# Performance work log

Hardware: AMD Instinct MI355X
Metric: run time of the kernel (lower is better)

## Reference

```python
import jax, jax.numpy as jnp
import numpy as np

EPS = 1e-5

def _conv3x3(x, w, b):
    y = jax.lax.conv_general_dilated(x, w, window_strides=(1, 1),
                                     padding=((1, 1), (1, 1)),
                                     dimension_numbers=('NCHW', 'OIHW', 'NCHW'))
    return y + b[None, :, None, None]

def _bilinear_gather(x, py, px):
    # x: [B,C,H,W]; py,px: [B,K,H,W] absolute sampling coords; zero outside image (DCN convention).
    B, C, H, W = x.shape
    Kk = py.shape[1]
    y0 = jnp.floor(py)
    x0 = jnp.floor(px)
    ly = py - y0
    lx = px - x0
    y0i = y0.astype(jnp.int32)
    x0i = x0.astype(jnp.int32)
    xf = x.reshape(B, C, H * W)

    def gather(yi, xi):
        valid = (yi >= 0) & (yi < H) & (xi >= 0) & (xi < W)
        idx = (jnp.clip(yi, 0, H - 1) * W + jnp.clip(xi, 0, W - 1)).reshape(B, -1)
        g = jax.vmap(lambda xb, ib: xb[:, ib])(xf, idx).reshape(B, C, Kk, H, W)
        return g * valid[:, None].astype(x.dtype)

    v00 = gather(y0i, x0i)
    v01 = gather(y0i, x0i + 1)
    v10 = gather(y0i + 1, x0i)
    v11 = gather(y0i + 1, x0i + 1)
    ly = ly[:, None]
    lx = lx[:, None]
    return (v00 * (1 - ly) * (1 - lx) + v01 * (1 - ly) * lx
            + v10 * ly * (1 - lx) + v11 * ly * lx)

def _shift_forward(x, w_off, b_off, w_conv, b_conv, gamma, beta, run_mean, run_var):
    B, C, H, W = x.shape
    om = _conv3x3(x, w_off, b_off)              # [B,27,H,W] offset/mask predictor
    dy = om[:, 0:18:2]                          # [B,9,H,W] per-tap y offsets
    dx = om[:, 1:18:2]                          # [B,9,H,W] per-tap x offsets
    mask = jax.nn.sigmoid(om[:, 18:27])         # [B,9,H,W] modulation (DCNv2)
    kk = jnp.arange(3, dtype=x.dtype) - 1.0     # kernel tap offsets for 3x3, dilation 1
    ky = jnp.repeat(kk, 3)                      # [9]
    kx = jnp.tile(kk, 3)                        # [9]
    hh = jnp.arange(H, dtype=x.dtype)
    ww = jnp.arange(W, dtype=x.dtype)
    py = hh[None, None, :, None] + ky[None, :, None, None] + dy
    px = ww[None, None, None, :] + kx[None, :, None, None] + dx
    s = _bilinear_gather(x, py, px) * mask[:, None]   # [B,C,9,H,W]
    Co = w_conv.shape[0]
    y = jnp.einsum('bckhw,ock->bohw', s, w_conv.reshape(Co, C, 9))
    y = y + b_conv[None, :, None, None]
    # BatchNorm2d (inference) + ReLU, then residual add
    inv = jax.lax.rsqrt(run_var + EPS)
    y = (y - run_mean[None, :, None, None]) * (inv * gamma)[None, :, None, None] + beta[None, :, None, None]
    y = jax.nn.relu(y)
    return x + y

def setup_inputs():
    key = jax.random.key(0)
    ks = jax.random.split(key, 3)
    B, C, H, W = 2, 256, 96, 96
    x = jax.random.normal(ks[0], (B, C, H, W), dtype=jnp.float32)
    w_off = jax.random.normal(ks[1], (27, C, 3, 3), dtype=jnp.float32) * 0.01
    b_off = jnp.zeros((27,), dtype=jnp.float32)
    w_conv = jax.random.normal(ks[2], (C, C, 3, 3), dtype=jnp.float32) * 0.02
    b_conv = jnp.zeros((C,), dtype=jnp.float32)
    gamma = jnp.ones((C,), dtype=jnp.float32)
    beta = jnp.zeros((C,), dtype=jnp.float32)
    run_mean = jnp.zeros((C,), dtype=jnp.float32)
    run_var = jnp.ones((C,), dtype=jnp.float32)
    return {"x": x, "w_off": w_off, "b_off": b_off, "w_conv": w_conv,
            "b_conv": b_conv, "gamma": gamma, "beta": beta,
            "run_mean": run_mean, "run_var": run_var}

def reference(x, w_off, b_off, w_conv, b_conv, gamma, beta, run_mean, run_var):
    return _shift_forward(x, w_off, b_off, w_conv, b_conv, gamma, beta, run_mean, run_var)
```

## Files before the change

### kernel.cpp

```cpp
#include <hip/hip_runtime.h>
#include <hip/hip_bf16.h>

#define H_ 96
#define W_ 96
#define HW_ 9216
#define C_ 256
#define B_ 2
#define KO_ 27
#define NPX_ 18432
#define EPS_ 1e-5f

typedef unsigned short u16;
typedef unsigned short ushort8 __attribute__((ext_vector_type(8)));
typedef short short8v __attribute__((ext_vector_type(8)));
typedef float float4v __attribute__((ext_vector_type(4)));

__device__ __forceinline__ float b2f(u16 u) {
    return __uint_as_float(((unsigned int)u) << 16);
}
__device__ __forceinline__ u16 f2b(float f) {
    __hip_bfloat16 h = __float2bfloat16(f);
    union { __hip_bfloat16 h; u16 u; } cv; cv.h = h; return cv.u;
}
__device__ __forceinline__ unsigned int pack2(float a, float b) {
    union { __hip_bfloat162 h; unsigned int u; } cv;
    cv.h = __float22bfloat162_rn(make_float2(a, b));
    return cv.u;
}
__device__ __forceinline__ void glds16(const u16* g, u16* l) {
    __builtin_amdgcn_global_load_lds(
        (const __attribute__((address_space(1))) void*)g,
        (__attribute__((address_space(3))) void*)l, 16, 0, 0);
}

__global__ __launch_bounds__(256) void prep_w_kernel(
    const float* __restrict__ w_conv, const float* __restrict__ w_off,
    const float* __restrict__ b_conv,
    const float* __restrict__ gamma, const float* __restrict__ beta,
    const float* __restrict__ rmean, const float* __restrict__ rvar,
    float* __restrict__ AB, u16* __restrict__ WQ, u16* __restrict__ WO)
{
    if (blockIdx.x == 0) {
        int o = threadIdx.x;
        float sc = gamma[o] * rsqrtf(rvar[o] + EPS_);
        AB[o] = sc;
        AB[256 + o] = beta[o] + (b_conv[o] - rmean[o]) * sc;
    }
    if (blockIdx.x < 2304) {
        int idx = blockIdx.x * 256 + threadIdx.x;
        int ch = idx >> 13;
        int o  = (idx >> 5) & 255;
        int cp = idx & 31;
        int c  = ((ch & 7) << 5) + cp;
        int k  = ch >> 3;
        WQ[idx] = f2b(w_conv[(o * C_ + c) * 9 + k]);
    } else {
        int j = (blockIdx.x - 2304) * 256 + threadIdx.x;
        int ch = j >> 10;
        int o  = (j >> 5) & 31;
        int cp = j & 31;
        int c  = ((ch & 7) << 5) + cp;
        int k  = ch >> 3;
        WO[j] = (o < KO_) ? f2b(w_off[(o * C_ + c) * 9 + k]) : (u16)0;
    }
}

__global__ __launch_bounds__(256) void xt_kernel(const float* __restrict__ x,
                                                 u16* __restrict__ XT)
{
    __shared__ u16 ls[32][100];
    int h  = blockIdx.x;
    int cg = blockIdx.y & 7;
    int b  = blockIdx.y >> 3;
    int c0 = cg * 32;
    for (int e = threadIdx.x; e < 32 * W_; e += 256) {
        int ci = e / W_, w = e % W_;
        ls[ci][w] = f2b(x[((b * C_ + c0 + ci) * H_ + h) * W_ + w]);
    }
    __syncthreads();
    for (int e = threadIdx.x; e < 32 * W_; e += 256) {
        int w = e >> 5, ci = e & 31;
        XT[((b * H_ + h) * W_ + w) * C_ + c0 + ci] = ls[ci][w];
    }
}

__global__ __launch_bounds__(256) void offsets_kernel(
    const u16* __restrict__ XT, const u16* __restrict__ WO,
    const float* __restrict__ b_off, float* __restrict__ OFF)
{
    __shared__ float red[4][32][16];

    const int tid = threadIdx.x;
    const int b  = blockIdx.y;
    const int p0 = blockIdx.x * 16;
    const int h  = p0 / W_;
    const int w0 = p0 % W_;

    const int wave = tid >> 6;
    const int lane = tid & 63;
    const int quad = lane >> 4;
    const int l15  = lane & 15;

    {
        const int pw = w0 + l15;
        float4v acc0 = float4v{0.f,0.f,0.f,0.f};
        float4v acc1 = float4v{0.f,0.f,0.f,0.f};
        int basec = 0; bool vld = true; int curtap = -1;
        auto set_tap = [&](int tap) {
            int py  = h + tap / 3 - 1;
            int pxl = pw + tap % 3 - 1;
            vld = ((unsigned)py < (unsigned)H_) && ((unsigned)pxl < (unsigned)W_);
            int pyc = min(max(py, 0), H_ - 1);
            int pxc = min(max(pxl, 0), W_ - 1);
            basec = ((b * H_ + pyc) * W_ + pxc) * C_ + quad * 8;
        };
        auto bload = [&](int c32) -> ushort8 {
            ushort8 v = *(const ushort8*)(XT + basec + (c32 & 7) * 32);
#pragma unroll
            for (int j = 0; j < 8; j++) v[j] = vld ? v[j] : (u16)0;
            return v;
        };
        const int c0 = wave * 18, c1 = c0 + 18;
        curtap = c0 >> 3;
        set_tap(curtap);
        ushort8 bq = bload(c0);
        short8v wa = *(const short8v*)(WO + c0 * 1024 + l15 * 32 + quad * 8);
        short8v wb = *(const short8v*)(WO + c0 * 1024 + l15 * 32 + quad * 8 + 512);
        for (int i = c0; i < c1; ++i) {
            ushort8 bc = bq;
            short8v wac = wa, wbc = wb;
            int nx = i + 1;
            if (nx < c1) {
                int t = nx >> 3;
                if (t != curtap) { set_tap(t); curtap = t; }
                bq = bload(nx);
                wa = *(const short8v*)(WO + nx * 1024 + l15 * 32 + quad * 8);
                wb = *(const short8v*)(WO + nx * 1024 + l15 * 32 + quad * 8 + 512);
            }
            union { ushort8 u; short8v s; } cb; cb.u = bc;
            acc0 = __builtin_amdgcn_mfma_f32_16x16x32_bf16(wac, cb.s, acc0, 0, 0, 0);
            acc1 = __builtin_amdgcn_mfma_f32_16x16x32_bf16(wbc, cb.s, acc1, 0, 0, 0);
        }
#pragma unroll
        for (int r = 0; r < 4; ++r) {
            red[wave][quad * 4 + r][l15]      = acc0[r];
            red[wave][16 + quad * 4 + r][l15] = acc1[r];
        }
    }
    __syncthreads();
    const int n_base = b * HW_ + p0;
#pragma unroll
    for (int rep = 0; rep < 2; ++rep) {
        int o  = (tid >> 4) + rep * 16;
        int px = tid & 15;
        if (o < KO_) {
            float v = red[0][o][px] + red[1][o][px] + red[2][o][px] + red[3][o][px]
                    + b_off[o];
            OFF[(size_t)(n_base + px) * 32 + o] =
                (o < 18) ? v : 1.f / (1.f + expf(-v));
        }
    }
}

__global__ __launch_bounds__(256) void fused_kernel(
    const float* __restrict__ x, const u16* __restrict__ XT,
    const float* __restrict__ OFF, const u16* __restrict__ WQ,
    const float* __restrict__ AB, float* __restrict__ out)
{
    __shared__ __align__(16) u16 sA[2 * 256 * 32];
    __shared__ __align__(16) u16 sB[2 * 32 * 32];
    __shared__ float offv[32][32];

    const int tid = threadIdx.x;
    const int wave = tid >> 6;
    const int lane = tid & 63;
    const int quad = lane >> 4;
    const int l15  = lane & 15;

    const int bid = blockIdx.x;
    const int swz = (bid & 7) * 72 + (bid >> 3);
    const int n0  = swz * 32;
    const int b   = n0 / HW_;
    const int p0  = n0 - b * HW_;
    const int h   = p0 / W_;
    const int w0  = p0 % W_;

    {
        int px = tid >> 3, q4 = (tid & 7) * 4;
        float4 v = *(const float4*)(OFF + (size_t)(n0 + px) * 32 + q4);
        *(float4*)&offv[px][q4] = v;
    }
    __syncthreads();

    float4v acc[4][2];
#pragma unroll
    for (int i = 0; i < 4; i++)
#pragma unroll
        for (int jj = 0; jj < 2; jj++)
            acc[i][jj] = float4v{0.f, 0.f, 0.f, 0.f};

    const int le8 = lane * 8;
    const int wo  = wave * 64;

    const int ppx = tid >> 3;
    const int pj  = tid & 7;
    const int pcc = pj >> 2;
    const int sboff = pcc * 1024 + ppx * 32 + (pj & 3) * 8;

    float fw0 = 0.f, fw1 = 0.f, fw2 = 0.f, fw3 = 0.f;
    int a00 = 0, a01 = 0, a10 = 0, a11 = 0;

#pragma unroll 4
    for (int ch = 0; ch < 36; ++ch) {
        const int tap = ch >> 2, q = ch & 3;
        if (q == 0) {
            float dy = offv[ppx][2 * tap];
            float dx = offv[ppx][2 * tap + 1];
            float m  = offv[ppx][18 + tap];
            float py  = (float)(h + tap / 3 - 1) + dy;
            float pxx = (float)(w0 + ppx + tap % 3 - 1) + dx;
            float y0f = floorf(py), x0f = floorf(pxx);
            float ly = py - y0f, lx = pxx - x0f;
            int y0 = (int)y0f, x0i = (int)x0f;
            int y1 = y0 + 1, x1 = x0i + 1;
            bool vy0 = (unsigned)y0 < (unsigned)H_;
            bool vy1 = (unsigned)y1 < (unsigned)H_;
            bool vx0 = (unsigned)x0i < (unsigned)W_;
            bool vx1 = (unsigned)x1 < (unsigned)W_;
            fw0 = (vy0 && vx0) ? (1.f - ly) * (1.f - lx) * m : 0.f;
            fw1 = (vy0 && vx1) ? (1.f - ly) * lx * m : 0.f;
            fw2 = (vy1 && vx0) ? ly * (1.f - lx) * m : 0.f;
            fw3 = (vy1 && vx1) ? ly * lx * m : 0.f;
            int y0c = min(max(y0, 0), H_ - 1), y1c = min(max(y1, 0), H_ - 1);
            int x0c = min(max(x0i, 0), W_ - 1), x1c = min(max(x1, 0), W_ - 1);
            a00 = ((b * H_ + y0c) * W_ + x0c) * C_;
            a01 = ((b * H_ + y0c) * W_ + x1c) * C_;
            a10 = ((b * H_ + y1c) * W_ + x0c) * C_;
            a11 = ((b * H_ + y1c) * W_ + x1c) * C_;
        }

        const int cbase = q * 64 + pj * 8;
        ushort8 v00 = *(const ushort8*)(XT + a00 + cbase);
        ushort8 v01 = *(const ushort8*)(XT + a01 + cbase);
        ushort8 v10 = *(const ushort8*)(XT + a10 + cbase);
        ushort8 v11 = *(const ushort8*)(XT + a11 + cbase);

#pragma unroll
        for (int i = 0; i < 8; ++i) {
            int unit = i * 4 + wave;
            int cc = unit >> 4;
            const u16* g = WQ + (size_t)(tap * 8 + q * 2 + cc) * 8192
                         + (unit & 15) * 512 + le8;
            glds16(g, &sA[unit * 512]);
        }

        {
            float v[8];
#pragma unroll
            for (int t = 0; t < 8; t++)
                v[t] = fw0 * b2f(v00[t]) + fw1 * b2f(v01[t])
                     + fw2 * b2f(v10[t]) + fw3 * b2f(v11[t]);
            uint4 sv;
            sv.x = pack2(v[0], v[1]);
            sv.y = pack2(v[2], v[3]);
            sv.z = pack2(v[4], v[5]);
            sv.w = pack2(v[6], v[7]);
            *(uint4*)&sB[sboff] = sv;
        }
        __syncthreads();

#pragma unroll
        for (int cc = 0; cc < 2; ++cc) {
            short8v af[4], bf[2];
#pragma unroll
            for (int mt = 0; mt < 4; ++mt)
                af[mt] = *(const short8v*)
                    &sA[cc * 8192 + (wo + mt * 16 + l15) * 32 + quad * 8];
#pragma unroll
            for (int nt = 0; nt < 2; ++nt)
                bf[nt] = *(const short8v*)
                    &sB[cc * 1024 + (nt * 16 + l15) * 32 + quad * 8];
#pragma unroll
            for (int mt = 0; mt < 4; ++mt)
#pragma unroll
                for (int nt = 0; nt < 2; ++nt)
                    acc[mt][nt] = __builtin_amdgcn_mfma_f32_16x16x32_bf16(
                        af[mt], bf[nt], acc[mt][nt], 0, 0, 0);
        }
        __syncthreads();
    }

    const float* Ao = AB;
    const float* Bo = AB + 256;
#pragma unroll
    for (int mt = 0; mt < 4; mt++) {
#pragma unroll
        for (int nt = 0; nt < 2; nt++) {
            int pix = p0 + nt * 16 + l15;
#pragma unroll
            for (int r = 0; r < 4; r++) {
                int o = wo + mt * 16 + quad * 4 + r;
                float v = acc[mt][nt][r] * Ao[o] + Bo[o];
                v = fmaxf(v, 0.f);
                int gi = (b * C_ + o) * HW_ + pix;
                out[gi] = x[gi] + v;
            }
        }
    }
}

extern "C" void kernel_launch(void* const* d_in, const int* in_sizes, int n_in,
                              void* d_out, int out_size, void* d_ws, size_t ws_size,
                              hipStream_t stream)
{
    (void)in_sizes; (void)n_in; (void)out_size; (void)ws_size;
    const float* x      = (const float*)d_in[0];
    const float* w_off  = (const float*)d_in[1];
    const float* b_off  = (const float*)d_in[2];
    const float* w_conv = (const float*)d_in[3];
    const float* b_conv = (const float*)d_in[4];
    const float* gamma  = (const float*)d_in[5];
    const float* beta   = (const float*)d_in[6];
    const float* rmean  = (const float*)d_in[7];
    const float* rvar   = (const float*)d_in[8];
    float* out = (float*)d_out;

    float* ws = (float*)d_ws;
    float* AB = ws;
    u16* WQ = (u16*)(AB + 512);
    u16* WO = WQ + 589824;
    u16* XT = WO + 73728;
    float* OFF = (float*)(XT + 4718592);

    prep_w_kernel<<<2592, 256, 0, stream>>>(w_conv, w_off, b_conv, gamma, beta,
                                            rmean, rvar, AB, WQ, WO);
    xt_kernel<<<dim3(96, 16), 256, 0, stream>>>(x, XT);
    offsets_kernel<<<dim3(576, 2), 256, 0, stream>>>(XT, WO, b_off, OFF);
    fused_kernel<<<576, 256, 0, stream>>>(x, XT, OFF, WQ, AB, out);
}
```

Baseline: 176.2 us.

## Software-pipeline gather and weight loads behind MFMA, swizzle LDS layout

The main loop is restructured so the next chunk's bilinear-tap gathers and weight global-to-LDS copies are issued after the fragments are read into registers and before the MFMAs. The intent is to overlap global memory latency with matrix math instead of stalling on it every iteration. An XOR swizzle is applied to the weight layout in the prep kernel and to both LDS read and write addresses to reduce bank conflicts. MFMA issue priority is also raised with s_setprio. Costs include more registers held live across the loop, which may lower occupancy, and reliance on hand-placed waitcnt and barrier instructions for correctness.

```diff
diff --git a/kernel.cpp b/kernel.cpp
--- a/kernel.cpp
+++ b/kernel.cpp
@@ -50,7 +50,8 @@
         int idx = blockIdx.x * 256 + threadIdx.x;
         int ch = idx >> 13;
         int o  = (idx >> 5) & 255;
-        int cp = idx & 31;
+        int cpa = idx & 31;
+        int cp  = cpa ^ ((o & 3) << 3);
         int c  = ((ch & 7) << 5) + cp;
         int k  = ch >> 3;
         WQ[idx] = f2b(w_conv[(o * C_ + c) * 9 + k]);
@@ -167,8 +168,8 @@
     const float* __restrict__ OFF, const u16* __restrict__ WQ,
     const float* __restrict__ AB, float* __restrict__ out)
 {
-    __shared__ __align__(16) u16 sA[2 * 256 * 32];
-    __shared__ __align__(16) u16 sB[2 * 32 * 32];
+    __shared__ __align__(16) u16 sA[16384];
+    __shared__ __align__(16) u16 sB[2048];
     __shared__ float offv[32][32];
 
     const int tid = threadIdx.x;
@@ -176,6 +177,7 @@
     const int lane = tid & 63;
     const int quad = lane >> 4;
     const int l15  = lane & 15;
+    const int qx   = (quad ^ (l15 & 3)) << 3;
 
     const int bid = blockIdx.x;
     const int swz = (bid & 7) * 72 + (bid >> 3);
@@ -204,62 +206,61 @@
 
     const int ppx = tid >> 3;
     const int pj  = tid & 7;
-    const int pcc = pj >> 2;
-    const int sboff = pcc * 1024 + ppx * 32 + (pj & 3) * 8;
-
-    float fw0 = 0.f, fw1 = 0.f, fw2 = 0.f, fw3 = 0.f;
-    int a00 = 0, a01 = 0, a10 = 0, a11 = 0;
+    const int sboff = (pj >> 2) * 1024 + ppx * 32
+                    + (((pj & 3) ^ (ppx & 3)) << 3);
+
+    float fn0, fn1, fn2, fn3;
+    int a00, a01, a10, a11;
+
+    auto tap_setup = [&](int tap) {
+        float dy = offv[ppx][2 * tap];
+        float dx = offv[ppx][2 * tap + 1];
+        float m  = offv[ppx][18 + tap];
+        float py  = (float)(h + tap / 3 - 1) + dy;
+        float pxx = (float)(w0 + ppx + tap % 3 - 1) + dx;
+        float y0f = floorf(py), x0f = floorf(pxx);
+        float ly = py - y0f, lx = pxx - x0f;
+        int y0 = (int)y0f, x0i = (int)x0f;
+        int y1 = y0 + 1, x1 = x0i + 1;
+        bool vy0 = (unsigned)y0 < (unsigned)H_;
+        bool vy1 = (unsigned)y1 < (unsigned)H_;
+        bool vx0 = (unsigned)x0i < (unsigned)W_;
+        bool vx1 = (unsigned)x1 < (unsigned)W_;
+        fn0 = (vy0 && vx0) ? (1.f - ly) * (1.f - lx) * m : 0.f;
+        fn1 = (vy0 && vx1) ? (1.f - ly) * lx * m : 0.f;
+        fn2 = (vy1 && vx0) ? ly * (1.f - lx) * m : 0.f;
+        fn3 = (vy1 && vx1) ? ly * lx * m : 0.f;
+        int y0c = min(max(y0, 0), H_ - 1), y1c = min(max(y1, 0), H_ - 1);
+        int x0c = min(max(x0i, 0), W_ - 1), x1c = min(max(x1, 0), W_ - 1);
+        a00 = ((b * H_ + y0c) * W_ + x0c) * C_;
+        a01 = ((b * H_ + y0c) * W_ + x1c) * C_;
+        a10 = ((b * H_ + y1c) * W_ + x0c) * C_;
+        a11 = ((b * H_ + y1c) * W_ + x1c) * C_;
+    };
+
+    tap_setup(0);
+    float fc0 = fn0, fc1 = fn1, fc2 = fn2, fc3 = fn3;
+    ushort8 gc00 = *(const ushort8*)(XT + a00 + pj * 8);
+    ushort8 gc01 = *(const ushort8*)(XT + a01 + pj * 8);
+    ushort8 gc10 = *(const ushort8*)(XT + a10 + pj * 8);
+    ushort8 gc11 = *(const ushort8*)(XT + a11 + pj * 8);
+#pragma unroll
+    for (int i = 0; i < 8; ++i) {
+        int unit = i * 4 + wave;
+        int cc = unit >> 4;
+        glds16(WQ + (size_t)cc * 8192 + (unit & 15) * 512 + le8,
+               &sA[unit * 512]);
+    }
+    ushort8 gn00{}, gn01{}, gn10{}, gn11{};
 
 #pragma unroll 4
     for (int ch = 0; ch < 36; ++ch) {
-        const int tap = ch >> 2, q = ch & 3;
-        if (q == 0) {
-            float dy = offv[ppx][2 * tap];
-            float dx = offv[ppx][2 * tap + 1];
-            float m  = offv[ppx][18 + tap];
-            float py  = (float)(h + tap / 3 - 1) + dy;
-            float pxx = (float)(w0 + ppx + tap % 3 - 1) + dx;
-            float y0f = floorf(py), x0f = floorf(pxx);
-            float ly = py - y0f, lx = pxx - x0f;
-            int y0 = (int)y0f, x0i = (int)x0f;
-            int y1 = y0 + 1, x1 = x0i + 1;
-            bool vy0 = (unsigned)y0 < (unsigned)H_;
-            bool vy1 = (unsigned)y1 < (unsigned)H_;
-            bool vx0 = (unsigned)x0i < (unsigned)W_;
-            bool vx1 = (unsigned)x1 < (unsigned)W_;
-            fw0 = (vy0 && vx0) ? (1.f - ly) * (1.f - lx) * m : 0.f;
-            fw1 = (vy0 && vx1) ? (1.f - ly) * lx * m : 0.f;
-            fw2 = (vy1 && vx0) ? ly * (1.f - lx) * m : 0.f;
-            fw3 = (vy1 && vx1) ? ly * lx * m : 0.f;
-            int y0c = min(max(y0, 0), H_ - 1), y1c = min(max(y1, 0), H_ - 1);
-            int x0c = min(max(x0i, 0), W_ - 1), x1c = min(max(x1, 0), W_ - 1);
-            a00 = ((b * H_ + y0c) * W_ + x0c) * C_;
-            a01 = ((b * H_ + y0c) * W_ + x1c) * C_;
-            a10 = ((b * H_ + y1c) * W_ + x0c) * C_;
-            a11 = ((b * H_ + y1c) * W_ + x1c) * C_;
-        }
-
-        const int cbase = q * 64 + pj * 8;
-        ushort8 v00 = *(const ushort8*)(XT + a00 + cbase);
-        ushort8 v01 = *(const ushort8*)(XT + a01 + cbase);
-        ushort8 v10 = *(const ushort8*)(XT + a10 + cbase);
-        ushort8 v11 = *(const ushort8*)(XT + a11 + cbase);
-
-#pragma unroll
-        for (int i = 0; i < 8; ++i) {
-            int unit = i * 4 + wave;
-            int cc = unit >> 4;
-            const u16* g = WQ + (size_t)(tap * 8 + q * 2 + cc) * 8192
-                         + (unit & 15) * 512 + le8;
-            glds16(g, &sA[unit * 512]);
-        }
-
         {
             float v[8];
 #pragma unroll
             for (int t = 0; t < 8; t++)
-                v[t] = fw0 * b2f(v00[t]) + fw1 * b2f(v01[t])
-                     + fw2 * b2f(v10[t]) + fw3 * b2f(v11[t]);
+                v[t] = fc0 * b2f(gc00[t]) + fc1 * b2f(gc01[t])
+                     + fc2 * b2f(gc10[t]) + fc3 * b2f(gc11[t]);
             uint4 sv;
             sv.x = pack2(v[0], v[1]);
             sv.y = pack2(v[2], v[3]);
@@ -267,27 +268,53 @@
             sv.w = pack2(v[6], v[7]);
             *(uint4*)&sB[sboff] = sv;
         }
-        __syncthreads();
-
+        asm volatile("s_waitcnt vmcnt(0) lgkmcnt(0)" ::: "memory");
+        __builtin_amdgcn_s_barrier();
+
+        short8v af[2][4], bfr[2][2];
 #pragma unroll
         for (int cc = 0; cc < 2; ++cc) {
-            short8v af[4], bf[2];
 #pragma unroll
             for (int mt = 0; mt < 4; ++mt)
-                af[mt] = *(const short8v*)
-                    &sA[cc * 8192 + (wo + mt * 16 + l15) * 32 + quad * 8];
+                af[cc][mt] = *(const short8v*)
+                    &sA[cc * 8192 + (wo + mt * 16 + l15) * 32 + qx];
 #pragma unroll
             for (int nt = 0; nt < 2; ++nt)
-                bf[nt] = *(const short8v*)
-                    &sB[cc * 1024 + (nt * 16 + l15) * 32 + quad * 8];
+                bfr[cc][nt] = *(const short8v*)
+                    &sB[cc * 1024 + (nt * 16 + l15) * 32 + qx];
+        }
+        asm volatile("s_waitcnt lgkmcnt(0)" ::: "memory");
+        __builtin_amdgcn_s_barrier();
+
+        if (ch < 35) {
+            const int chn = ch + 1, tapn = chn >> 2, qn = chn & 3;
+            if (qn == 0) tap_setup(tapn);
+            const int cb = qn * 64 + pj * 8;
+            gn00 = *(const ushort8*)(XT + a00 + cb);
+            gn01 = *(const ushort8*)(XT + a01 + cb);
+            gn10 = *(const ushort8*)(XT + a10 + cb);
+            gn11 = *(const ushort8*)(XT + a11 + cb);
+#pragma unroll
+            for (int i = 0; i < 8; ++i) {
+                int unit = i * 4 + wave;
+                int cc = unit >> 4;
+                glds16(WQ + (size_t)(tapn * 8 + qn * 2 + cc) * 8192
+                          + (unit & 15) * 512 + le8,
+                       &sA[unit * 512]);
+            }
+        }
+        __builtin_amdgcn_s_setprio(1);
+#pragma unroll
+        for (int cc = 0; cc < 2; ++cc)
 #pragma unroll
             for (int mt = 0; mt < 4; ++mt)
 #pragma unroll
                 for (int nt = 0; nt < 2; ++nt)
                     acc[mt][nt] = __builtin_amdgcn_mfma_f32_16x16x32_bf16(
-                        af[mt], bf[nt], acc[mt][nt], 0, 0, 0);
-        }
-        __syncthreads();
+                        af[cc][mt], bfr[cc][nt], acc[mt][nt], 0, 0, 0);
+        __builtin_amdgcn_s_setprio(0);
+        gc00 = gn00; gc01 = gn01; gc10 = gn10; gc11 = gn11;
+        fc0 = fn0; fc1 = fn1; fc2 = fn2; fc3 = fn3;
     }
 
     const float* Ao = AB;
```

New measurement: 177.6 us. No clear change (+0.8%).
